# Kernel tuning notes

Hardware: AMD Instinct MI355X
Metric: run time of the kernel (lower is better)

Reference implementation:

```python
import jax, jax.numpy as jnp
import numpy as np

N_NODES = 65536
N_EDGES = 524288
N_GRAPHS = 64
PTS_PER_GRAPH = 1024


def gcn_conv(x, W, b, row, col, self_idx, n_nodes):
    # PyG GCNConv: x' = D^{-1/2} (A + I) D^{-1/2} x W + b
    xw = x @ W
    row2 = jnp.concatenate([row, self_idx])
    col2 = jnp.concatenate([col, self_idx])
    deg = jax.ops.segment_sum(jnp.ones_like(col2, dtype=xw.dtype), col2, num_segments=n_nodes)
    dinv = jax.lax.rsqrt(deg)  # deg >= 1 thanks to self-loops
    norm = dinv[row2] * dinv[col2]  # [E+N]
    out = jax.ops.segment_sum(xw[row2] * norm[:, None], col2, num_segments=n_nodes)
    return out + b


def setup_inputs() -> dict:
    key = jax.random.key(0)
    ks = jax.random.split(key, 12)

    def glorot(k, fan_in, fan_out):
        s = jnp.sqrt(6.0 / (fan_in + fan_out))
        return jax.random.uniform(k, (fan_in, fan_out), jnp.float32, -s, s)

    x = jax.random.normal(ks[0], (N_NODES, 3), jnp.float32)
    edge_index = jax.random.randint(ks[1], (2, N_EDGES), 0, N_NODES, dtype=jnp.int64)
    batch = (jnp.arange(N_NODES, dtype=jnp.int64) // PTS_PER_GRAPH)  # 64 graphs x 1024 pts

    return {
        "x": x, "edge_index": edge_index, "batch": batch,
        "W1": glorot(ks[2], 3, 64), "b1": jnp.zeros((64,), jnp.float32),
        "W2": glorot(ks[3], 64, 256), "b2": jnp.zeros((256,), jnp.float32),
        "W3": glorot(ks[4], 256, 512), "b3": jnp.zeros((512,), jnp.float32),
        "Wm1": glorot(ks[5], 1024, 512), "bm1": jnp.zeros((512,), jnp.float32),
        "Wm2": glorot(ks[6], 512, 10), "bm2": jnp.zeros((10,), jnp.float32),
    }


def reference(x, edge_index, batch, W1, b1, W2, b2, W3, b3, Wm1, bm1, Wm2, bm2):
    n = x.shape[0]
    row, col = edge_index[0], edge_index[1]
    self_idx = jnp.arange(n, dtype=edge_index.dtype)

    x1 = jax.nn.relu(gcn_conv(x, W1, b1, row, col, self_idx, n))
    x2 = jax.nn.relu(gcn_conv(x1, W2, b2, row, col, self_idx, n))
    x3 = jax.nn.relu(gcn_conv(x2, W3, b3, row, col, self_idx, n))

    # global mean / max pool over batch segments
    counts = jax.ops.segment_sum(jnp.ones((n,), x3.dtype), batch, num_segments=N_GRAPHS)
    x_mean = jax.ops.segment_sum(x3, batch, num_segments=N_GRAPHS) / counts[:, None]
    x_max = jax.ops.segment_max(x3, batch, num_segments=N_GRAPHS)
    h = jnp.concatenate([x_mean, x_max], axis=1)  # [G, 1024]

    h = jax.nn.relu(h @ Wm1 + bm1)  # dropout is identity in eval
    return h @ Wm2 + bm2  # [G, 10]
```

## Files before the change

kernel.cpp:

```cpp
#include <hip/hip_runtime.h>
#include <hip/hip_bf16.h>

typedef __hip_bfloat16 bf16;
typedef short bf16x8 __attribute__((ext_vector_type(8)));
typedef float f32x4 __attribute__((ext_vector_type(4)));
typedef unsigned int u32x4 __attribute__((ext_vector_type(4)));

__device__ __forceinline__ float b2f_us(unsigned short u) {
    union { unsigned int i; float f; } c;
    c.i = ((unsigned int)u) << 16;
    return c.f;
}
__device__ __forceinline__ unsigned short f2b_us(float f) {
    bf16 h = __float2bfloat16(f);
    return *reinterpret_cast<unsigned short*>(&h);
}
__device__ __forceinline__ void unpack8(uint4 p, float* f) {
    f[0] = b2f_us(p.x & 0xffff); f[1] = b2f_us(p.x >> 16);
    f[2] = b2f_us(p.y & 0xffff); f[3] = b2f_us(p.y >> 16);
    f[4] = b2f_us(p.z & 0xffff); f[5] = b2f_us(p.z >> 16);
    f[6] = b2f_us(p.w & 0xffff); f[7] = b2f_us(p.w >> 16);
}

__device__ __forceinline__ void async_copy16(const bf16* g, bf16* l) {
    __builtin_amdgcn_global_load_lds(
        (const __attribute__((address_space(1))) unsigned int*)g,
        (__attribute__((address_space(3))) unsigned int*)l, 16, 0, 0);
}

__global__ __launch_bounds__(256) void k_count(const int* __restrict__ col,
                                               int* __restrict__ cnt,
                                               int* __restrict__ rank, int E) {
    int e = blockIdx.x * 256 + threadIdx.x;
    if (e < E) rank[e] = atomicAdd(cnt + col[e], 1);
}
__global__ __launch_bounds__(256) void k_scan_a(const int* __restrict__ cnt,
                                                int* __restrict__ bsum,
                                                float* __restrict__ dinv) {
    __shared__ int s[256];
    int t = threadIdx.x;
    int i = blockIdx.x * 256 + t;
    int c = cnt[i];
    dinv[i] = rsqrtf((float)c + 1.0f);
    s[t] = c;
    __syncthreads();
#pragma unroll
    for (int off = 128; off >= 1; off >>= 1) {
        if (t < off) s[t] += s[t + off];
        __syncthreads();
    }
    if (t == 0) bsum[blockIdx.x] = s[0];
}
__global__ __launch_bounds__(256) void k_scan_c(const int* __restrict__ cnt,
                                                const int* __restrict__ bsum,
                                                int* __restrict__ rowptr) {
    __shared__ int s[256];
    __shared__ int sb[256];
    int t = threadIdx.x;
    sb[t] = bsum[t];
    __syncthreads();
#pragma unroll
    for (int off = 1; off < 256; off <<= 1) {
        int v = (t >= off) ? sb[t - off] : 0;
        __syncthreads();
        sb[t] += v;
        __syncthreads();
    }
    int boff = (blockIdx.x > 0) ? sb[blockIdx.x - 1] : 0;
    int base = blockIdx.x * 256;
    int self = cnt[base + t];
    s[t] = self;
    __syncthreads();
#pragma unroll
    for (int off = 1; off < 256; off <<= 1) {
        int v = (t >= off) ? s[t - off] : 0;
        __syncthreads();
        s[t] += v;
        __syncthreads();
    }
    rowptr[base + t] = boff + s[t] - self;
}

__global__ __launch_bounds__(256) void k_scatter(const int* __restrict__ row,
                                                 const int* __restrict__ col,
                                                 const float* __restrict__ dinv,
                                                 const int* __restrict__ rowptr,
                                                 const int* __restrict__ rank,
                                                 int2* __restrict__ adj, int E) {
    int e = blockIdx.x * 256 + threadIdx.x;
    if (e >= E) return;
    int r = row[e], c = col[e];
    int pos = rowptr[c] + rank[e];
    adj[pos] = make_int2(r, __float_as_int(dinv[r]));
}

__global__ __launch_bounds__(256) void k_prep_all(const float* __restrict__ W2,
                                                  bf16* __restrict__ WT2,
                                                  const float* __restrict__ W3,
                                                  bf16* __restrict__ WT3) {
    int idx = blockIdx.x * 256 + threadIdx.x;
    if (idx < 64 * 256) {
        int k = idx >> 8, n = idx & 255;
        WT2[n * 64 + k] = __float2bfloat16(W2[idx]);
    } else {
        int i = idx - 64 * 256;
        if (i < 256 * 512) {
            int k = i >> 9, n = i & 511;
            WT3[(size_t)n * 256 + k] = __float2bfloat16(W3[i]);
        }
    }
}

__global__ __launch_bounds__(256) void k_gcn1(const int2* __restrict__ adj,
                                              const int* __restrict__ rowptr,
                                              const int* __restrict__ cnt,
                                              const float* __restrict__ dinv,
                                              const float* __restrict__ x,
                                              const float* __restrict__ W,
                                              const float* __restrict__ bias,
                                              bf16* __restrict__ h1, int N) {
    __shared__ float w[256];
    int t = threadIdx.x;
    if (t < 192) w[t] = W[t];
    else w[t] = bias[t - 192];
    __syncthreads();
    int node = blockIdx.x * 64 + (t >> 2);
    int q = t & 3;
    if (node >= N) return;
    float d = dinv[node];
    float a0 = 0.f, a1 = 0.f, a2 = 0.f;
    if (q == 0) {
        float d2 = d * d;
        a0 = x[node * 3] * d2;
        a1 = x[node * 3 + 1] * d2;
        a2 = x[node * 3 + 2] * d2;
    }
    int beg = rowptr[node], deg = cnt[node];
    int e   = beg + (deg * q) / 4;
    int end = beg + (deg * (q + 1)) / 4;
    for (; e + 3 < end; e += 4) {
        int2 ad[4];
#pragma unroll
        for (int u = 0; u < 4; ++u) ad[u] = adj[e + u];
        float xv[4][3];
#pragma unroll
        for (int u = 0; u < 4; ++u) {
            xv[u][0] = x[ad[u].x * 3];
            xv[u][1] = x[ad[u].x * 3 + 1];
            xv[u][2] = x[ad[u].x * 3 + 2];
        }
#pragma unroll
        for (int u = 0; u < 4; ++u) {
            float wt = __int_as_float(ad[u].y) * d;
            a0 += xv[u][0] * wt;
            a1 += xv[u][1] * wt;
            a2 += xv[u][2] * wt;
        }
    }
    for (; e < end; ++e) {
        int2 ad = adj[e];
        float wt = __int_as_float(ad.y) * d;
        a0 += x[ad.x * 3] * wt;
        a1 += x[ad.x * 3 + 1] * wt;
        a2 += x[ad.x * 3 + 2] * wt;
    }
    a0 += __shfl_xor(a0, 1); a1 += __shfl_xor(a1, 1); a2 += __shfl_xor(a2, 1);
    a0 += __shfl_xor(a0, 2); a1 += __shfl_xor(a1, 2); a2 += __shfl_xor(a2, 2);
    bf16* dst = h1 + (size_t)node * 64;
#pragma unroll
    for (int i = 0; i < 2; ++i) {
        int fb = q + 4 * i;
        uint4 r;
        unsigned v[4];
#pragma unroll
        for (int p = 0; p < 4; ++p) {
            int f0 = fb * 8 + p * 2;
            float u0 = fmaxf(a0 * w[f0] + a1 * w[64 + f0] + a2 * w[128 + f0] + w[192 + f0], 0.f);
            int f1 = f0 + 1;
            float u1 = fmaxf(a0 * w[f1] + a1 * w[64 + f1] + a2 * w[128 + f1] + w[192 + f1], 0.f);
            v[p] = (unsigned)f2b_us(u0) | ((unsigned)f2b_us(u1) << 16);
        }
        r.x = v[0]; r.y = v[1]; r.z = v[2]; r.w = v[3];
        *reinterpret_cast<uint4*>(dst + fb * 8) = r;
    }
}

template <int F>
__global__ __launch_bounds__(256, 8) void k_gather_pre(const int2* __restrict__ adj,
                                                       const int* __restrict__ rowptr,
                                                       const int* __restrict__ cnt,
                                                       const float* __restrict__ dinv,
                                                       const bf16* __restrict__ h,
                                                       bf16* __restrict__ agg, int N) {
    constexpr int LPN = F / 8;
    constexpr int GRP = 2 * LPN;
    constexpr int NPB = 256 / GRP;
    int t = threadIdx.x;
    int node = blockIdx.x * NPB + t / GRP;
    if (node >= N) return;
    int gl = t % GRP;
    int fs = gl % LPN;
    int half = gl / LPN;
    int fbase = fs * 8;
    float d = dinv[node];
    size_t sbase = (size_t)node * F + fbase;
    float a[8] = {0.f, 0.f, 0.f, 0.f, 0.f, 0.f, 0.f, 0.f};
    if (half == 0) {
        uint4 sp = *reinterpret_cast<const uint4*>(h + sbase);
        unpack8(sp, a);
        float d2 = d * d;
#pragma unroll
        for (int i = 0; i < 8; i++) a[i] *= d2;
    }
    int beg = rowptr[node];
    int deg = cnt[node];
    int mid = beg + ((deg + 1) >> 1);
    int e   = half ? mid : beg;
    int end = half ? (beg + deg) : mid;
    for (; e + 3 < end; e += 4) {
        int2 ad[4];
        uint4 p[4];
#pragma unroll
        for (int u = 0; u < 4; ++u) ad[u] = adj[e + u];
#pragma unroll
        for (int u = 0; u < 4; ++u)
            p[u] = *reinterpret_cast<const uint4*>(h + (size_t)ad[u].x * F + fbase);
#pragma unroll
        for (int u = 0; u < 4; ++u) {
            float wt = __int_as_float(ad[u].y) * d;
            float f[8];
            unpack8(p[u], f);
#pragma unroll
            for (int i = 0; i < 8; i++) a[i] += f[i] * wt;
        }
    }
    for (; e < end; ++e) {
        int2 ad = adj[e];
        float wt = __int_as_float(ad.y) * d;
        uint4 p = *reinterpret_cast<const uint4*>(h + (size_t)ad.x * F + fbase);
        float f[8];
        unpack8(p, f);
#pragma unroll
        for (int i = 0; i < 8; i++) a[i] += f[i] * wt;
    }
#pragma unroll
    for (int i = 0; i < 8; i++) a[i] += __shfl_xor(a[i], LPN);
    if (half == 0) {
        u32x4 r;
        r.x = (unsigned)f2b_us(a[0]) | ((unsigned)f2b_us(a[1]) << 16);
        r.y = (unsigned)f2b_us(a[2]) | ((unsigned)f2b_us(a[3]) << 16);
        r.z = (unsigned)f2b_us(a[4]) | ((unsigned)f2b_us(a[5]) << 16);
        r.w = (unsigned)f2b_us(a[6]) | ((unsigned)f2b_us(a[7]) << 16);
        __builtin_nontemporal_store(r, reinterpret_cast<u32x4*>(agg + sbase));
    }
}

__global__ __launch_bounds__(256) void k_gemm_br(const bf16* __restrict__ A,
                                                 const bf16* __restrict__ BT,
                                                 const float* __restrict__ bias,
                                                 bf16* __restrict__ C,
                                                 int M, int N, int K) {
    __shared__ bf16 As[128 * 32];
    __shared__ bf16 Bs[128 * 32];
    const int t = threadIdx.x;
    const int wave = t >> 6, lane = t & 63;
    const int quad = lane >> 4, l16 = lane & 15;
    const int wm = wave & 1, wn = wave >> 1;
    const int L = blockIdx.x;
    const int xcd = L & 7, slot = L >> 3;
    const int mt = xcd * 64 + (slot >> 1), nt = slot & 1;
    const int m0 = mt * 128;
    const int n0 = nt * 128;

    f32x4 acc[4][4] = {};
    for (int kb = 0; kb < K; kb += 32) {
#pragma unroll
        for (int rnd = 0; rnd < 2; ++rnd) {
            int c = (rnd * 4 + wave) * 64 + lane;
            int r = c >> 2, seg = c & 3;
            async_copy16(A + (size_t)(m0 + r) * K + kb + seg * 8, As + c * 8);
            async_copy16(BT + (size_t)(n0 + r) * K + kb + seg * 8, Bs + c * 8);
        }
        __syncthreads();
        bf16x8 af[4], bfr[4];
#pragma unroll
        for (int i = 0; i < 4; i++)
            af[i] = *reinterpret_cast<const bf16x8*>(&As[(wm * 64 + i * 16 + l16) * 32 + quad * 8]);
#pragma unroll
        for (int j = 0; j < 4; j++)
            bfr[j] = *reinterpret_cast<const bf16x8*>(&Bs[(wn * 64 + j * 16 + l16) * 32 + quad * 8]);
#pragma unroll
        for (int i = 0; i < 4; i++)
#pragma unroll
            for (int j = 0; j < 4; j++)
                acc[i][j] = __builtin_amdgcn_mfma_f32_16x16x32_bf16(af[i], bfr[j], acc[i][j], 0, 0, 0);
        __syncthreads();
    }
#pragma unroll
    for (int j = 0; j < 4; j++) {
        int cn = n0 + wn * 64 + j * 16 + l16;
        float bv = bias[cn];
#pragma unroll
        for (int i = 0; i < 4; i++) {
            int row = m0 + wm * 64 + i * 16 + quad * 4;
#pragma unroll
            for (int r = 0; r < 4; r++)
                C[(size_t)(row + r) * N + cn] = __float2bfloat16(fmaxf(acc[i][j][r] + bv, 0.f));
        }
    }
}

__global__ __launch_bounds__(256) void k_gemm_pool(const bf16* __restrict__ A,
                                                   const bf16* __restrict__ BT,
                                                   const float* __restrict__ bias,
                                                   float* __restrict__ partials,
                                                   int M, int N, int K) {
    __shared__ bf16 As[128 * 32];
    __shared__ bf16 Bs[128 * 32];
    const int t = threadIdx.x;
    const int wave = t >> 6, lane = t & 63;
    const int quad = lane >> 4, l16 = lane & 15;
    const int wm = wave & 1, wn = wave >> 1;
    const int L = blockIdx.x;
    const int xcd = L & 7, slot = L >> 3;
    const int mt = xcd * 64 + (slot >> 2), nt = slot & 3;
    const int m0 = mt * 128;
    const int n0 = nt * 128;

    f32x4 acc[4][4] = {};
    for (int kb = 0; kb < K; kb += 32) {
#pragma unroll
        for (int rnd = 0; rnd < 2; ++rnd) {
            int c = (rnd * 4 + wave) * 64 + lane;
            int r = c >> 2, seg = c & 3;
            async_copy16(A + (size_t)(m0 + r) * K + kb + seg * 8, As + c * 8);
            async_copy16(BT + (size_t)(n0 + r) * K + kb + seg * 8, Bs + c * 8);
        }
        __syncthreads();
        bf16x8 af[4], bfr[4];
#pragma unroll
        for (int i = 0; i < 4; i++)
            af[i] = *reinterpret_cast<const bf16x8*>(&As[(wm * 64 + i * 16 + l16) * 32 + quad * 8]);
#pragma unroll
        for (int j = 0; j < 4; j++)
            bfr[j] = *reinterpret_cast<const bf16x8*>(&Bs[(wn * 64 + j * 16 + l16) * 32 + quad * 8]);
#pragma unroll
        for (int i = 0; i < 4; i++)
#pragma unroll
            for (int j = 0; j < 4; j++)
                acc[i][j] = __builtin_amdgcn_mfma_f32_16x16x32_bf16(af[i], bfr[j], acc[i][j], 0, 0, 0);
        __syncthreads();
    }
    size_t pbase = ((size_t)(mt * 4 + nt) * 2 + wm) * 256;
#pragma unroll
    for (int j = 0; j < 4; j++) {
        int f128 = wn * 64 + j * 16 + l16;
        float bv = bias[n0 + f128];
        float s = 0.f, mx = 0.f;
#pragma unroll
        for (int i = 0; i < 4; i++)
#pragma unroll
            for (int r = 0; r < 4; r++) {
                float v = fmaxf(acc[i][j][r] + bv, 0.f);
                s += v;
                mx = fmaxf(mx, v);
            }
        s += __shfl_xor(s, 16);
        s += __shfl_xor(s, 32);
        mx = fmaxf(mx, __shfl_xor(mx, 16));
        mx = fmaxf(mx, __shfl_xor(mx, 32));
        if (quad == 0) {
            partials[pbase + f128] = s;
            partials[pbase + 128 + f128] = mx;
        }
    }
}

__global__ __launch_bounds__(256) void k_mlp1(const float* __restrict__ partials,
                                              const float* __restrict__ Wm1,
                                              const float* __restrict__ bm1,
                                              float* __restrict__ o) {
    __shared__ float hg[1024];
    __shared__ float red[256];
    int g = blockIdx.x;
    int t = threadIdx.x;
    for (int ff = t; ff < 512; ff += 256) {
        int by = ff >> 7, f128 = ff & 127;
        float S = 0.f, M = 0.f;
#pragma unroll
        for (int tile = 0; tile < 8; ++tile) {
            int bx = g * 8 + tile;
#pragma unroll
            for (int wm = 0; wm < 2; ++wm) {
                size_t pbase = ((size_t)(bx * 4 + by) * 2 + wm) * 256;
                S += partials[pbase + f128];
                M = fmaxf(M, partials[pbase + 128 + f128]);
            }
        }
        hg[ff] = S * (1.0f / 1024.0f);
        hg[512 + ff] = M;
    }
    __syncthreads();
    int f64 = t & 63, kq = t >> 6;
    int f = blockIdx.y * 64 + f64;
    float acc = 0.f;
    int k0 = kq * 256;
#pragma unroll 8
    for (int k = k0; k < k0 + 256; ++k)
        acc += hg[k] * Wm1[(size_t)k * 512 + f];
    red[t] = acc;
    __syncthreads();
    if (t < 64) {
        float total = red[t] + red[t + 64] + red[t + 128] + red[t + 192] + bm1[f];
        o[g * 512 + f] = fmaxf(total, 0.f);
    }
}

__global__ __launch_bounds__(512) void k_mlp2(const float* __restrict__ h,
                                              const float* __restrict__ Wm2,
                                              const float* __restrict__ bm2,
                                              float* __restrict__ out) {
    int g = blockIdx.x;
    int t = threadIdx.x;
    int j = t >> 5, lane32 = t & 31;
    float acc = 0.f;
    if (j < 10) {
        int k0 = lane32 * 16;
#pragma unroll
        for (int i = 0; i < 16; ++i)
            acc += h[g * 512 + k0 + i] * Wm2[(size_t)(k0 + i) * 10 + j];
    }
#pragma unroll
    for (int m = 16; m >= 1; m >>= 1) acc += __shfl_xor(acc, m);
    if (j < 10 && lane32 == 0) out[g * 10 + j] = acc + bm2[j];
}

extern "C" void kernel_launch(void* const* d_in, const int* in_sizes, int n_in,
                              void* d_out, int out_size, void* d_ws, size_t ws_size,
                              hipStream_t stream) {
    const float* x   = (const float*)d_in[0];
    const int*   ei  = (const int*)d_in[1];
    const float* W1  = (const float*)d_in[3];
    const float* b1  = (const float*)d_in[4];
    const float* W2  = (const float*)d_in[5];
    const float* b2  = (const float*)d_in[6];
    const float* W3  = (const float*)d_in[7];
    const float* b3  = (const float*)d_in[8];
    const float* Wm1 = (const float*)d_in[9];
    const float* bm1 = (const float*)d_in[10];
    const float* Wm2 = (const float*)d_in[11];
    const float* bm2 = (const float*)d_in[12];
    float* out = (float*)d_out;

    const int N = in_sizes[0] / 3;
    const int E = in_sizes[1] / 2;
    const int* row = ei;
    const int* col = ei + E;

    char* ws = (char*)d_ws;
    size_t off = 0;
    auto alloc = [&](size_t bytes) {
        void* p = ws + off;
        off += (bytes + 255) & ~(size_t)255;
        return p;
    };
    int*   cnt      = (int*)alloc((size_t)N * 4);
    int*   rowptr   = (int*)alloc((size_t)N * 4);
    float* dinv     = (float*)alloc((size_t)N * 4);
    int*   bsum     = (int*)alloc(256 * 4);
    int*   rank     = (int*)alloc((size_t)E * 4);
    int2*  adj      = (int2*)alloc((size_t)E * 8);
    bf16*  h1       = (bf16*)alloc((size_t)N * 64 * 2);
    bf16*  agg2     = (bf16*)alloc((size_t)N * 64 * 2);
    bf16*  h2       = (bf16*)alloc((size_t)N * 256 * 2);
    bf16*  agg3     = (bf16*)alloc((size_t)N * 256 * 2);
    bf16*  WT2      = (bf16*)alloc(256 * 64 * 2);
    bf16*  WT3      = (bf16*)alloc(512 * 256 * 2);
    float* partials = (float*)alloc((size_t)512 * 4 * 2 * 256 * 4);
    float* m1       = (float*)alloc(64 * 512 * 4);

    (void)hipMemsetAsync(cnt, 0, (size_t)N * 4, stream);
    k_count<<<(E + 255) / 256, 256, 0, stream>>>(col, cnt, rank, E);
    k_scan_a<<<256, 256, 0, stream>>>(cnt, bsum, dinv);
    k_scan_c<<<256, 256, 0, stream>>>(cnt, bsum, rowptr);
    k_scatter<<<(E + 255) / 256, 256, 0, stream>>>(row, col, dinv, rowptr, rank, adj, E);

    k_prep_all<<<(64 * 256 + 256 * 512 + 255) / 256, 256, 0, stream>>>(W2, WT2, W3, WT3);

    k_gcn1<<<N / 64, 256, 0, stream>>>(adj, rowptr, cnt, dinv, x, W1, b1, h1, N);

    k_gather_pre<64><<<(N * 16) / 256, 256, 0, stream>>>(adj, rowptr, cnt, dinv, h1, agg2, N);
    k_gemm_br<<<(N / 128) * 2, 256, 0, stream>>>(agg2, WT2, b2, h2, N, 256, 64);

    k_gather_pre<256><<<(N * 64) / 256, 256, 0, stream>>>(adj, rowptr, cnt, dinv, h2, agg3, N);
    k_gemm_pool<<<(N / 128) * 4, 256, 0, stream>>>(agg3, WT3, b3, partials, N, 512, 256);

    k_mlp1<<<dim3(64, 8), 256, 0, stream>>>(partials, Wm1, bm1, m1);
    k_mlp2<<<64, 512, 0, stream>>>(m1, Wm2, bm2, out);
}
```

Before: 252.9 us.

## Fuse layer-2 neighbor aggregation with the 64x256 MFMA GEMM in one kernel

Replaces the separate layer-2 gather kernel and the bf16 GEMM with a single kernel. Each 512-thread block aggregates 64 nodes' neighbor features into swizzled shared memory, loads the whole transposed W2 into LDS, and runs the MFMA GEMM with bias and ReLU. This drops the agg2 intermediate round trip through global memory and one launch. In exchange it uses a larger LDS footprint per block (40KB) and gives the gather phase less parallelism per block, which may limit occupancy.

```diff
diff --git a/kernel.cpp b/kernel.cpp
--- a/kernel.cpp
+++ b/kernel.cpp
@@ -182,6 +182,114 @@
         }
         r.x = v[0]; r.y = v[1]; r.z = v[2]; r.w = v[3];
         *reinterpret_cast<uint4*>(dst + fb * 8) = r;
+    }
+}
+
+__global__ __launch_bounds__(512, 4) void k_gcn2(const int2* __restrict__ adj,
+                                                 const int* __restrict__ rowptr,
+                                                 const int* __restrict__ cnt,
+                                                 const float* __restrict__ dinv,
+                                                 const bf16* __restrict__ h1,
+                                                 const bf16* __restrict__ WT2,
+                                                 const float* __restrict__ bias,
+                                                 bf16* __restrict__ h2, int N) {
+    __shared__ bf16 As[64 * 64];
+    __shared__ bf16 Bs[256 * 64];
+    const int t = threadIdx.x;
+    const int m0 = blockIdx.x * 64;
+#pragma unroll
+    for (int i = 0; i < 4; ++i) {
+        int c = i * 512 + t;
+        int n = c >> 3, q = c & 7;
+        int qs = q ^ (n & 7);
+        async_copy16(WT2 + n * 64 + qs * 8, Bs + c * 8);
+    }
+    {
+        const int gi = t >> 4, gl = t & 15;
+        const int fs = gl & 7, half = gl >> 3;
+        const int fbase = fs * 8;
+#pragma unroll 1
+        for (int p = 0; p < 2; ++p) {
+            int r = p * 32 + gi;
+            int node = m0 + r;
+            float d = dinv[node];
+            float a[8] = {0.f, 0.f, 0.f, 0.f, 0.f, 0.f, 0.f, 0.f};
+            if (half == 0) {
+                uint4 sp = *reinterpret_cast<const uint4*>(h1 + (size_t)node * 64 + fbase);
+                unpack8(sp, a);
+                float d2 = d * d;
+#pragma unroll
+                for (int i = 0; i < 8; i++) a[i] *= d2;
+            }
+            int beg = rowptr[node], deg = cnt[node];
+            int mid = beg + ((deg + 1) >> 1);
+            int e = half ? mid : beg;
+            int end = half ? (beg + deg) : mid;
+            for (; e + 3 < end; e += 4) {
+                int2 ad[4];
+                uint4 pl[4];
+#pragma unroll
+                for (int u = 0; u < 4; ++u) ad[u] = adj[e + u];
+#pragma unroll
+                for (int u = 0; u < 4; ++u)
+                    pl[u] = *reinterpret_cast<const uint4*>(h1 + (size_t)ad[u].x * 64 + fbase);
+#pragma unroll
+                for (int u = 0; u < 4; ++u) {
+                    float wt = __int_as_float(ad[u].y) * d;
+                    float f[8];
+                    unpack8(pl[u], f);
+#pragma unroll
+                    for (int i = 0; i < 8; i++) a[i] += f[i] * wt;
+                }
+            }
+            for (; e < end; ++e) {
+                int2 ad = adj[e];
+                float wt = __int_as_float(ad.y) * d;
+                uint4 pl = *reinterpret_cast<const uint4*>(h1 + (size_t)ad.x * 64 + fbase);
+                float f[8];
+                unpack8(pl, f);
+#pragma unroll
+                for (int i = 0; i < 8; i++) a[i] += f[i] * wt;
+            }
+#pragma unroll
+            for (int i = 0; i < 8; i++) a[i] += __shfl_xor(a[i], 8);
+            if (half == 0) {
+                u32x4 rr;
+                rr.x = (unsigned)f2b_us(a[0]) | ((unsigned)f2b_us(a[1]) << 16);
+                rr.y = (unsigned)f2b_us(a[2]) | ((unsigned)f2b_us(a[3]) << 16);
+                rr.z = (unsigned)f2b_us(a[4]) | ((unsigned)f2b_us(a[5]) << 16);
+                rr.w = (unsigned)f2b_us(a[6]) | ((unsigned)f2b_us(a[7]) << 16);
+                int q = fs ^ (r & 7);
+                *reinterpret_cast<u32x4*>(&As[r * 64 + q * 8]) = rr;
+            }
+        }
+    }
+    __syncthreads();
+    const int w = t >> 6, lane = t & 63;
+    const int quad = lane >> 4, l16 = lane & 15;
+    const int wmq = w & 3, wnh = w >> 2;
+    f32x4 acc[8] = {};
+#pragma unroll
+    for (int kb = 0; kb < 2; ++kb) {
+        int R = wmq * 16 + l16;
+        int kc = kb * 4 + quad;
+        bf16x8 af = *reinterpret_cast<const bf16x8*>(&As[R * 64 + (kc ^ (R & 7)) * 8]);
+#pragma unroll
+        for (int j = 0; j < 8; ++j) {
+            int n = wnh * 128 + j * 16 + l16;
+            bf16x8 bfr = *reinterpret_cast<const bf16x8*>(&Bs[n * 64 + (kc ^ (n & 7)) * 8]);
+            acc[j] = __builtin_amdgcn_mfma_f32_16x16x32_bf16(af, bfr, acc[j], 0, 0, 0);
+        }
+    }
+#pragma unroll
+    for (int j = 0; j < 8; ++j) {
+        int cn = wnh * 128 + j * 16 + l16;
+        float bv = bias[cn];
+#pragma unroll
+        for (int r = 0; r < 4; ++r) {
+            int row = m0 + wmq * 16 + quad * 4 + r;
+            h2[(size_t)row * 256 + cn] = __float2bfloat16(fmaxf(acc[j][r] + bv, 0.f));
+        }
     }
 }
 
@@ -255,61 +363,6 @@
     }
 }
 
-__global__ __launch_bounds__(256) void k_gemm_br(const bf16* __restrict__ A,
-                                                 const bf16* __restrict__ BT,
-                                                 const float* __restrict__ bias,
-                                                 bf16* __restrict__ C,
-                                                 int M, int N, int K) {
-    __shared__ bf16 As[128 * 32];
-    __shared__ bf16 Bs[128 * 32];
-    const int t = threadIdx.x;
-    const int wave = t >> 6, lane = t & 63;
-    const int quad = lane >> 4, l16 = lane & 15;
-    const int wm = wave & 1, wn = wave >> 1;
-    const int L = blockIdx.x;
-    const int xcd = L & 7, slot = L >> 3;
-    const int mt = xcd * 64 + (slot >> 1), nt = slot & 1;
-    const int m0 = mt * 128;
-    const int n0 = nt * 128;
-
-    f32x4 acc[4][4] = {};
-    for (int kb = 0; kb < K; kb += 32) {
-#pragma unroll
-        for (int rnd = 0; rnd < 2; ++rnd) {
-            int c = (rnd * 4 + wave) * 64 + lane;
-            int r = c >> 2, seg = c & 3;
-            async_copy16(A + (size_t)(m0 + r) * K + kb + seg * 8, As + c * 8);
-            async_copy16(BT + (size_t)(n0 + r) * K + kb + seg * 8, Bs + c * 8);
-        }
-        __syncthreads();
-        bf16x8 af[4], bfr[4];
-#pragma unroll
-        for (int i = 0; i < 4; i++)
-            af[i] = *reinterpret_cast<const bf16x8*>(&As[(wm * 64 + i * 16 + l16) * 32 + quad * 8]);
-#pragma unroll
-        for (int j = 0; j < 4; j++)
-            bfr[j] = *reinterpret_cast<const bf16x8*>(&Bs[(wn * 64 + j * 16 + l16) * 32 + quad * 8]);
-#pragma unroll
-        for (int i = 0; i < 4; i++)
-#pragma unroll
-            for (int j = 0; j < 4; j++)
-                acc[i][j] = __builtin_amdgcn_mfma_f32_16x16x32_bf16(af[i], bfr[j], acc[i][j], 0, 0, 0);
-        __syncthreads();
-    }
-#pragma unroll
-    for (int j = 0; j < 4; j++) {
-        int cn = n0 + wn * 64 + j * 16 + l16;
-        float bv = bias[cn];
-#pragma unroll
-        for (int i = 0; i < 4; i++) {
-            int row = m0 + wm * 64 + i * 16 + quad * 4;
-#pragma unroll
-            for (int r = 0; r < 4; r++)
-                C[(size_t)(row + r) * N + cn] = __float2bfloat16(fmaxf(acc[i][j][r] + bv, 0.f));
-        }
-    }
-}
-
 __global__ __launch_bounds__(256) void k_gemm_pool(const bf16* __restrict__ A,
                                                    const bf16* __restrict__ BT,
                                                    const float* __restrict__ bias,
@@ -471,7 +524,6 @@
     int*   rank     = (int*)alloc((size_t)E * 4);
     int2*  adj      = (int2*)alloc((size_t)E * 8);
     bf16*  h1       = (bf16*)alloc((size_t)N * 64 * 2);
-    bf16*  agg2     = (bf16*)alloc((size_t)N * 64 * 2);
     bf16*  h2       = (bf16*)alloc((size_t)N * 256 * 2);
     bf16*  agg3     = (bf16*)alloc((size_t)N * 256 * 2);
     bf16*  WT2      = (bf16*)alloc(256 * 64 * 2);
@@ -489,8 +541,7 @@
 
     k_gcn1<<<N / 64, 256, 0, stream>>>(adj, rowptr, cnt, dinv, x, W1, b1, h1, N);
 
-    k_gather_pre<64><<<(N * 16) / 256, 256, 0, stream>>>(adj, rowptr, cnt, dinv, h1, agg2, N);
-    k_gemm_br<<<(N / 128) * 2, 256, 0, stream>>>(agg2, WT2, b2, h2, N, 256, 64);
+    k_gcn2<<<N / 64, 512, 0, stream>>>(adj, rowptr, cnt, dinv, h1, WT2, b2, h2, N);
 
     k_gather_pre<256><<<(N * 64) / 256, 256, 0, stream>>>(adj, rowptr, cnt, dinv, h2, agg3, N);
     k_gemm_pool<<<(N / 128) * 4, 256, 0, stream>>>(agg3, WT3, b3, partials, N, 512, 256);
```

After: 245.9 us. 1.03x faster.
